# Kernel tuning notes

Measured on AMD Instinct MI355X. Metric: run time of the kernel, lower is better.

Reference implementation:

```python
import jax, jax.numpy as jnp
import numpy as np

B, L, V = 128, 48, 32000
NUM_BRANCHES, BRANCH_SIZE = 16, 8  # branch_nums = [8]*16, sum == B


def setup_inputs() -> dict:
    key = jax.random.key(0)
    k1, k2 = jax.random.split(key)
    tgt_tokens = jax.random.randint(k1, (B, L), 0, V, dtype=jnp.int32)
    pred = jax.random.normal(k2, (B, L, V), dtype=jnp.float32)
    # segment id per sample, encoding branch_nums = [BRANCH_SIZE]*NUM_BRANCHES
    seg_ids = jnp.repeat(jnp.arange(NUM_BRANCHES, dtype=jnp.int32), BRANCH_SIZE)
    return {"tgt_tokens": tgt_tokens, "pred": pred, "seg_ids": seg_ids}


def reference(tgt_tokens, pred, seg_ids):
    # batched cross-entropy with ignore_index=-100 (mean over valid tokens per sample)
    logp = jax.nn.log_softmax(pred, axis=-1)                      # [B, L, V]
    valid = tgt_tokens != -100                                    # [B, L]
    tok = jnp.where(valid, tgt_tokens, 0)
    nll = -jnp.take_along_axis(logp, tok[..., None], axis=-1)[..., 0]
    nll = jnp.where(valid, nll, 0.0)
    count = valid.sum(axis=-1).astype(pred.dtype)                 # valid tokens per sample
    ce_losses = nll.sum(axis=-1) / count                          # [B]
    # seq_probs[i] = exp(-count_i * ce_i) == exp(sum of token log-probs)
    seq_probs = jnp.exp(-count * ce_losses)                       # [B] (detached in original)
    # per-branch: -log(mean(exp(-ce)))  == -(logsumexp(-ce) - log(branch_num))
    neg = -ce_losses
    m = jax.ops.segment_max(neg, seg_ids, num_segments=NUM_BRANCHES)
    s = jax.ops.segment_sum(jnp.exp(neg - m[seg_ids]), seg_ids, num_segments=NUM_BRANCHES)
    cnt = jax.ops.segment_sum(jnp.ones_like(neg), seg_ids, num_segments=NUM_BRANCHES)
    branch_loss = -(jnp.log(s) + m - jnp.log(cnt))                # [NUM_BRANCHES]
    loss = jnp.mean(branch_loss)
    return loss, jax.lax.stop_gradient(seq_probs)
```

## Files before the change

kernel.cpp:

```cpp
#include <hip/hip_runtime.h>
#include <math.h>

#define BB 128
#define LL 48
#define VV 32000
#define NSEG 16

typedef float v4f __attribute__((ext_vector_type(4)));

__global__ __launch_bounds__(256) void row_nll_kernel(
    const int* __restrict__ tgt, const float* __restrict__ pred,
    float* __restrict__ nll_ws)
{
    const int wave = threadIdx.x >> 6;
    const int lane = threadIdx.x & 63;
    const int row  = blockIdx.x * 4 + wave;
    const float* __restrict__ p = pred + (size_t)row * VV;

    const int t = tgt[row];
    const float tlogit = (t != -100) ? p[t] : 0.0f;

    const v4f* __restrict__ p4 = (const v4f*)p;
    float s0 = 0.0f, s1 = 0.0f, s2 = 0.0f, s3 = 0.0f;
    #pragma unroll 5
    for (int i = lane; i < VV / 4; i += 64) {
        v4f v = __builtin_nontemporal_load(&p4[i]);
        s0 += __expf(v.x);
        s1 += __expf(v.y);
        s2 += __expf(v.z);
        s3 += __expf(v.w);
    }
    float s = (s0 + s1) + (s2 + s3);

    #pragma unroll
    for (int off = 1; off < 64; off <<= 1)
        s += __shfl_xor(s, off);

    if (lane == 0) {
        float nll = 0.0f;
        if (t != -100) nll = logf(s) - tlogit;
        nll_ws[row] = nll;
    }
}

__global__ __launch_bounds__(128) void finalize_kernel(
    const int* __restrict__ tgt, const int* __restrict__ seg_ids,
    const float* __restrict__ nll_ws, float* __restrict__ out)
{
    const int b = threadIdx.x;

    float sum = 0.0f; int count = 0;
    for (int l = 0; l < LL; l++) {
        sum += nll_ws[b * LL + l];
        if (tgt[b * LL + l] != -100) count++;
    }
    float ce = sum / (float)count;
    out[1 + b] = expf(-sum);

    __shared__ float neg[BB];
    __shared__ int   seg[BB];
    __shared__ float bl[NSEG];
    neg[b] = -ce;
    seg[b] = seg_ids[b];
    __syncthreads();

    if (b < NSEG) {
        float m = -INFINITY;
        for (int i = 0; i < BB; i++)
            if (seg[i] == b) m = fmaxf(m, neg[i]);
        float s = 0.0f; int cnt = 0;
        for (int i = 0; i < BB; i++)
            if (seg[i] == b) { s += expf(neg[i] - m); cnt++; }
        bl[b] = -(logf(s) + m - logf((float)cnt));
    }
    __syncthreads();

    if (b == 0) {
        float loss = 0.0f;
        for (int i = 0; i < NSEG; i++) loss += bl[i];
        out[0] = loss / (float)NSEG;
    }
}

extern "C" void kernel_launch(void* const* d_in, const int* in_sizes, int n_in,
                              void* d_out, int out_size, void* d_ws, size_t ws_size,
                              hipStream_t stream) {
    const int*   tgt  = (const int*)d_in[0];
    const float* pred = (const float*)d_in[1];
    const int*   seg  = (const int*)d_in[2];
    float* out    = (float*)d_out;
    float* nll_ws = (float*)d_ws;

    row_nll_kernel<<<(BB * LL) / 4, 256, 0, stream>>>(tgt, pred, nll_ws);
    finalize_kernel<<<1, BB, 0, stream>>>(tgt, seg, nll_ws, out);
}
```

Baseline: 145.9 us.

## Fuse finalize into row kernel via last-block atomic ticket

```diff
diff --git a/kernel.cpp b/kernel.cpp
--- a/kernel.cpp
+++ b/kernel.cpp
@@ -5,12 +5,14 @@
 #define LL 48
 #define VV 32000
 #define NSEG 16
+#define GRID ((BB * LL) / 4)
 
 typedef float v4f __attribute__((ext_vector_type(4)));
 
-__global__ __launch_bounds__(256) void row_nll_kernel(
+__global__ __launch_bounds__(256) void fused_kernel(
     const int* __restrict__ tgt, const float* __restrict__ pred,
-    float* __restrict__ nll_ws)
+    const int* __restrict__ seg_ids, float* __restrict__ out,
+    float* __restrict__ nll_ws, unsigned int* __restrict__ counter)
 {
     const int wave = threadIdx.x >> 6;
     const int lane = threadIdx.x & 63;
@@ -24,7 +26,7 @@
     float s0 = 0.0f, s1 = 0.0f, s2 = 0.0f, s3 = 0.0f;
     #pragma unroll 5
     for (int i = lane; i < VV / 4; i += 64) {
-        v4f v = __builtin_nontemporal_load(&p4[i]);
+        v4f v = p4[i];
         s0 += __expf(v.x);
         s1 += __expf(v.y);
         s2 += __expf(v.z);
@@ -37,41 +39,45 @@
         s += __shfl_xor(s, off);
 
     if (lane == 0) {
-        float nll = 0.0f;
-        if (t != -100) nll = logf(s) - tlogit;
+        float nll = (t != -100) ? (logf(s) - tlogit) : 0.0f;
         nll_ws[row] = nll;
     }
-}
 
-__global__ __launch_bounds__(128) void finalize_kernel(
-    const int* __restrict__ tgt, const int* __restrict__ seg_ids,
-    const float* __restrict__ nll_ws, float* __restrict__ out)
-{
+    __shared__ unsigned int ticket;
+    __syncthreads();
+    if (threadIdx.x == 0) {
+        __threadfence();
+        ticket = atomicAdd(counter, 1u);
+    }
+    __syncthreads();
+    if (ticket != GRID - 1) return;
+    __threadfence();
+
     const int b = threadIdx.x;
-
-    float sum = 0.0f; int count = 0;
-    for (int l = 0; l < LL; l++) {
-        sum += nll_ws[b * LL + l];
-        if (tgt[b * LL + l] != -100) count++;
-    }
-    float ce = sum / (float)count;
-    out[1 + b] = expf(-sum);
-
     __shared__ float neg[BB];
     __shared__ int   seg[BB];
     __shared__ float bl[NSEG];
-    neg[b] = -ce;
-    seg[b] = seg_ids[b];
+
+    if (b < BB) {
+        float sum = 0.0f; int count = 0;
+        for (int l = 0; l < LL; l++) {
+            sum += nll_ws[b * LL + l];
+            if (tgt[b * LL + l] != -100) count++;
+        }
+        out[1 + b] = expf(-sum);
+        neg[b] = -(sum / (float)count);
+        seg[b] = seg_ids[b];
+    }
     __syncthreads();
 
     if (b < NSEG) {
         float m = -INFINITY;
         for (int i = 0; i < BB; i++)
             if (seg[i] == b) m = fmaxf(m, neg[i]);
-        float s = 0.0f; int cnt = 0;
+        float ssum = 0.0f; int cnt = 0;
         for (int i = 0; i < BB; i++)
-            if (seg[i] == b) { s += expf(neg[i] - m); cnt++; }
-        bl[b] = -(logf(s) + m - logf((float)cnt));
+            if (seg[i] == b) { ssum += expf(neg[i] - m); cnt++; }
+        bl[b] = -(logf(ssum) + m - logf((float)cnt));
     }
     __syncthreads();
 
@@ -90,7 +96,8 @@
     const int*   seg  = (const int*)d_in[2];
     float* out    = (float*)d_out;
     float* nll_ws = (float*)d_ws;
+    unsigned int* counter = (unsigned int*)((char*)d_ws + (size_t)BB * LL * 4);
 
-    row_nll_kernel<<<(BB * LL) / 4, 256, 0, stream>>>(tgt, pred, nll_ws);
-    finalize_kernel<<<1, BB, 0, stream>>>(tgt, seg, nll_ws, out);
+    hipMemsetAsync(counter, 0, sizeof(unsigned int), stream);
+    fused_kernel<<<GRID, 256, 0, stream>>>(tgt, pred, seg, out, nll_ws, counter);
 }
```

Result: slower. 235.8 us (+61.6%).

## Split each row across two waves and stage finalize inputs in shared memory

Applied to the files above, without the earlier changes.

```diff
diff --git a/kernel.cpp b/kernel.cpp
--- a/kernel.cpp
+++ b/kernel.cpp
@@ -8,13 +8,14 @@
 
 typedef float v4f __attribute__((ext_vector_type(4)));
 
-__global__ __launch_bounds__(256) void row_nll_kernel(
+__global__ __launch_bounds__(256, 8) void row_nll_kernel(
     const int* __restrict__ tgt, const float* __restrict__ pred,
     float* __restrict__ nll_ws)
 {
     const int wave = threadIdx.x >> 6;
     const int lane = threadIdx.x & 63;
-    const int row  = blockIdx.x * 4 + wave;
+    const int row  = blockIdx.x * 2 + (wave >> 1);
+    const int half = wave & 1;
     const float* __restrict__ p = pred + (size_t)row * VV;
 
     const int t = tgt[row];
@@ -22,8 +23,8 @@
 
     const v4f* __restrict__ p4 = (const v4f*)p;
     float s0 = 0.0f, s1 = 0.0f, s2 = 0.0f, s3 = 0.0f;
-    #pragma unroll 5
-    for (int i = lane; i < VV / 4; i += 64) {
+    #pragma unroll 4
+    for (int i = lane + 64 * half; i < VV / 4; i += 128) {
         v4f v = __builtin_nontemporal_load(&p4[i]);
         s0 += __expf(v.x);
         s1 += __expf(v.y);
@@ -36,10 +37,13 @@
     for (int off = 1; off < 64; off <<= 1)
         s += __shfl_xor(s, off);
 
-    if (lane == 0) {
-        float nll = 0.0f;
-        if (t != -100) nll = logf(s) - tlogit;
-        nll_ws[row] = nll;
+    __shared__ float sw[4];
+    if (lane == 0) sw[wave] = s;
+    __syncthreads();
+
+    if (lane == 0 && half == 0) {
+        float tot = sw[wave] + sw[wave + 1];
+        nll_ws[row] = (t != -100) ? (logf(tot) - tlogit) : 0.0f;
     }
 }
 
@@ -49,10 +53,18 @@
 {
     const int b = threadIdx.x;
 
+    __shared__ float nl[BB * LL];
+    __shared__ int   tg[BB * LL];
+    for (int idx = b; idx < BB * LL; idx += 128) {
+        nl[idx] = nll_ws[idx];
+        tg[idx] = tgt[idx];
+    }
+    __syncthreads();
+
     float sum = 0.0f; int count = 0;
     for (int l = 0; l < LL; l++) {
-        sum += nll_ws[b * LL + l];
-        if (tgt[b * LL + l] != -100) count++;
+        sum += nl[b * LL + l];
+        if (tg[b * LL + l] != -100) count++;
     }
     float ce = sum / (float)count;
     out[1 + b] = expf(-sum);
@@ -68,10 +80,10 @@
         float m = -INFINITY;
         for (int i = 0; i < BB; i++)
             if (seg[i] == b) m = fmaxf(m, neg[i]);
-        float s = 0.0f; int cnt = 0;
+        float ssum = 0.0f; int cnt = 0;
         for (int i = 0; i < BB; i++)
-            if (seg[i] == b) { s += expf(neg[i] - m); cnt++; }
-        bl[b] = -(logf(s) + m - logf((float)cnt));
+            if (seg[i] == b) { ssum += expf(neg[i] - m); cnt++; }
+        bl[b] = -(logf(ssum) + m - logf((float)cnt));
     }
     __syncthreads();
 
@@ -91,6 +103,6 @@
     float* out    = (float*)d_out;
     float* nll_ws = (float*)d_ws;
 
-    row_nll_kernel<<<(BB * LL) / 4, 256, 0, stream>>>(tgt, pred, nll_ws);
+    row_nll_kernel<<<(BB * LL) / 2, 256, 0, stream>>>(tgt, pred, nll_ws);
     finalize_kernel<<<1, BB, 0, stream>>>(tgt, seg, nll_ws, out);
 }
```

Result: no change. 147.2 us (+0.9%).
